# Optimization experiments

Hardware: AMD Instinct MI355X
Metric: run time of the kernel (lower is better)

The kernel has to match this reference:

```python
import jax, jax.numpy as jnp
import numpy as np
import math

B, NQ, NS, K = 4, 4096, 16384, 16
P, IN, D = 3, 128, 256
H = D // 16   # nhead = out_dim // 16 = 16
HD = D // H   # head_dim = 16
RADIUS = 4.0
EPS = 1e-5


def _ln(x, g, b):
    m = jnp.mean(x, -1, keepdims=True)
    v = jnp.mean((x - m) ** 2, -1, keepdims=True)
    return (x - m) / jnp.sqrt(v + EPS) * g + b


def _pos_enc(x, W_pos, b_pos):
    # LearnablePositionalEncoding: cat([x, cos(Linear(2*pi*x))], -1)
    return jnp.concatenate([x, jnp.cos((2.0 * math.pi * x) @ W_pos + b_pos)], axis=-1)


def setup_inputs() -> dict:
    key = jax.random.key(0)
    ks = jax.random.split(key, 24)
    f32 = jnp.float32

    def w(k, shape):
        return jax.random.uniform(k, shape, f32, -1.0, 1.0) / np.float32(np.sqrt(shape[0]))

    inp = {}
    inp['q_pts'] = jax.random.normal(ks[0], (B, NQ, P), f32)
    inp['s_pts'] = jax.random.normal(ks[1], (B, NS, P), f32)
    inp['src_feats'] = jax.random.normal(ks[2], (B, NS, IN), f32)
    inp['query_feats'] = jax.random.normal(ks[3], (B, NQ, IN), f32)
    # shared proj (in_dim != out_dim, skip_dim=None -> skip_proj is the same Linear)
    inp['W_proj'] = w(ks[4], (IN, D)); inp['b_proj'] = jnp.zeros((D,), f32)
    # positional encoding Linear(p_dim, out_dim - p_dim)
    inp['W_pos'] = w(ks[5], (P, D - P)); inp['b_pos'] = jnp.zeros((D - P,), f32)
    # TransformerDecoderLayer (norm_first) params
    inp['ln1_g'] = jnp.ones((D,), f32); inp['ln1_b'] = jnp.zeros((D,), f32)
    inp['sa_Wv'] = w(ks[6], (D, D)); inp['sa_bv'] = jnp.zeros((D,), f32)
    inp['sa_Wo'] = w(ks[7], (D, D)); inp['sa_bo'] = jnp.zeros((D,), f32)
    inp['ln2_g'] = jnp.ones((D,), f32); inp['ln2_b'] = jnp.zeros((D,), f32)
    inp['ca_Wq'] = w(ks[8], (D, D)); inp['ca_bq'] = jnp.zeros((D,), f32)
    inp['ca_Wk'] = w(ks[9], (D, D)); inp['ca_bk'] = jnp.zeros((D,), f32)
    inp['ca_Wv'] = w(ks[10], (D, D)); inp['ca_bv'] = jnp.zeros((D,), f32)
    inp['ca_Wo'] = w(ks[11], (D, D)); inp['ca_bo'] = jnp.zeros((D,), f32)
    inp['ln3_g'] = jnp.ones((D,), f32); inp['ln3_b'] = jnp.zeros((D,), f32)
    inp['W1'] = w(ks[12], (D, D)); inp['b1'] = jnp.zeros((D,), f32)
    inp['W2'] = w(ks[13], (D, D)); inp['b2'] = jnp.zeros((D,), f32)
    inp['neighb_inds'] = jax.random.randint(ks[14], (B, NQ, K), 0, NS)
    return inp


def reference(q_pts, s_pts, src_feats, query_feats, W_proj, b_proj, W_pos, b_pos,
              ln1_g, ln1_b, sa_Wv, sa_bv, sa_Wo, sa_bo, ln2_g, ln2_b,
              ca_Wq, ca_bq, ca_Wk, ca_bk, ca_Wv, ca_bv, ca_Wo, ca_bo,
              ln3_g, ln3_b, W1, b1, W2, b2, neighb_inds):
    # append shadow point at 1e6 with zero feature row
    s_pts_ = jnp.concatenate([s_pts, jnp.full_like(s_pts[:, :1, :], 1e6)], axis=1)   # [B,NS+1,P]
    src_ = jnp.concatenate([src_feats, jnp.zeros_like(src_feats[:, :1, :])], axis=1)  # [B,NS+1,IN]
    src_p = src_ @ W_proj + b_proj            # proj(src_feats)  [B,NS+1,D]
    qf = query_feats @ W_proj + b_proj        # skip_proj == proj (skip_dim=None)
    inds = neighb_inds % (NS + 1)
    flat = inds.reshape(B, -1, 1)             # [B, NQ*K, 1]
    neighbors = jnp.take_along_axis(s_pts_, jnp.broadcast_to(flat, (B, NQ * K, P)), axis=1).reshape(B, NQ, K, P)
    neighb_x = jnp.take_along_axis(src_p, jnp.broadcast_to(flat, (B, NQ * K, D)), axis=1).reshape(B, NQ, K, D)
    neighbors = neighbors - q_pts[:, :, None, :]
    neighb_x = neighb_x + _pos_enc(neighbors / RADIUS, W_pos, b_pos)
    query_x = qf + _pos_enc(jnp.zeros_like(q_pts), W_pos, b_pos)
    mask = jnp.linalg.norm(neighbors, axis=-1) > RADIUS   # [B,NQ,K], True = invalid key

    x = query_x   # [B,NQ,D]: a length-1 target sequence per query point
    # --- self-attention block (seq len 1 -> softmax == 1 -> only V/O projections matter) ---
    h = _ln(x, ln1_g, ln1_b)
    x = x + (h @ sa_Wv + sa_bv) @ sa_Wo + sa_bo
    # --- cross-attention to K gathered neighbors ---
    h = _ln(x, ln2_g, ln2_b)
    q = (h @ ca_Wq + ca_bq).reshape(B, NQ, H, HD)
    kk = (neighb_x @ ca_Wk + ca_bk).reshape(B, NQ, K, H, HD)
    vv = (neighb_x @ ca_Wv + ca_bv).reshape(B, NQ, K, H, HD)
    scores = jnp.einsum('bnhd,bnkhd->bnhk', q, kk) / np.float32(np.sqrt(HD))
    scores = jnp.where(mask[:, :, None, :], jnp.float32(-1e9), scores)
    att = jax.nn.softmax(scores, axis=-1)
    ctx = jnp.einsum('bnhk,bnkhd->bnhd', att, vv).reshape(B, NQ, D)
    x = x + ctx @ ca_Wo + ca_bo
    # --- feed-forward (dim_feedforward == d_model, relu) ---
    h = _ln(x, ln3_g, ln3_b)
    x = x + jax.nn.relu(h @ W1 + b1) @ W2 + b2
    # original zeroes any NaNs (fully-masked rows); shapes chosen so this is a no-op
    return jnp.nan_to_num(x)
```

## Files before the change

kernel.cpp:

```cpp
#include <hip/hip_runtime.h>
#include <hip/hip_bf16.h>
#include <math.h>
#include <stdint.h>

typedef __attribute__((ext_vector_type(8))) short short8;
typedef __attribute__((ext_vector_type(4))) float floatx4;

#define DEVI __device__ __forceinline__

DEVI float b2f(unsigned short u) {
    union { unsigned int i; float f; } v; v.i = ((unsigned int)u) << 16; return v.f;
}
DEVI unsigned short f2b(float f) {
    unsigned int x = __float_as_uint(f);
    unsigned int r = (x + 0x7fffu + ((x >> 16) & 1u)) >> 16;
    return (unsigned short)r;
}

#define GLD16(gp, lp)                                                            \
    __builtin_amdgcn_global_load_lds(                                            \
        (__attribute__((address_space(1))) unsigned int*)(gp),                   \
        (__attribute__((address_space(3))) unsigned int*)(lp), 16, 0, 0)

static constexpr int NQ = 4096, NS = 16384;
static constexpr int NROW_Q = 4 * NQ;
static constexpr int NROW_S = 4 * NS;
static constexpr float INV2PI = 0.15915494309189535f;

__global__ void k_prep(const float* Wproj, const float* saWv, const float* saWo,
                       const float* caWq, const float* caWk, const float* caWv,
                       const float* caWo, const float* W1, const float* W2,
                       const float* b_pos,
                       unsigned short* wTproj, unsigned short* wTsaWv, unsigned short* wTsaWo,
                       unsigned short* wTcaWq, unsigned short* wTkv, unsigned short* wTcaWo,
                       unsigned short* wTW1, unsigned short* wTW2, float* penc0)
{
    int z = blockIdx.z;
    if (z == 9) {
        if (blockIdx.x == 0 && blockIdx.y == 0) {
            int c = threadIdx.y * 16 + threadIdx.x;
            float v = 0.f;
            if (c >= 3) {
                float rev = b_pos[c - 3] * INV2PI;
                rev -= floorf(rev);
                v = __builtin_amdgcn_cosf(rev);
            }
            penc0[c] = v;
        }
        return;
    }
    int n = blockIdx.x * 16 + threadIdx.x;
    int k = blockIdx.y * 16 + threadIdx.y;
    const float* src; unsigned short* dst; int K = 256;
    switch (z) {
        case 0: src = Wproj; dst = wTproj; K = 128; break;
        case 1: src = saWv;  dst = wTsaWv; break;
        case 2: src = saWo;  dst = wTsaWo; break;
        case 3: src = caWq;  dst = wTcaWq; break;
        case 4: src = caWk;  dst = wTkv;   break;
        case 5: src = caWv;  dst = wTkv + 256 * 256; break;
        case 6: src = caWo;  dst = wTcaWo; break;
        case 7: src = W1;    dst = wTW1;   break;
        default: src = W2;   dst = wTW2;   break;
    }
    if (k < K) dst[(size_t)n * K + k] = f2b(src[(size_t)k * 256 + n]);
}

__global__ void k_cvt(const float* in, unsigned short* out, int n4)
{
    int i = blockIdx.x * blockDim.x + threadIdx.x;
    int stride = gridDim.x * blockDim.x;
    for (; i < n4; i += stride) {
        float4 v = ((const float4*)in)[i];
        unsigned long long p =
              (unsigned long long)f2b(v.x)
            | ((unsigned long long)f2b(v.y) << 16)
            | ((unsigned long long)f2b(v.z) << 32)
            | ((unsigned long long)f2b(v.w) << 48);
        ((unsigned long long*)out)[i] = p;
    }
}

template<int EPI>
__global__ __launch_bounds__(256, 2)
void k_gemm(const unsigned short* A, const unsigned short* BT, const float* bias,
            const float* extra, void* outp, int M, int N, int K)
{
    __shared__ alignas(16) unsigned short lA[128 * 64];
    __shared__ alignas(16) unsigned short lB[64 * 64];
    const int tid = threadIdx.x;
    const int wave = tid >> 6, lane = tid & 63;
    const int m0 = blockIdx.x * 128, n0 = blockIdx.y * 64;
    const int wm = (wave >> 1) * 64, wn = (wave & 1) * 32;
    floatx4 acc[4][2] = {};

    for (int kt = 0; kt < K; kt += 64) {
        __syncthreads();
        #pragma unroll
        for (int c = 0; c < 4; ++c) {
            int o = (tid + c * 256) * 16;
            int row = o >> 7, inner = o & 127;
            int srk = inner ^ ((row & 7) << 4);
            GLD16((const char*)A + ((size_t)(m0 + row) * K + kt) * 2 + srk, (char*)lA + o);
        }
        #pragma unroll
        for (int c = 0; c < 2; ++c) {
            int o = (tid + c * 256) * 16;
            int row = o >> 7, inner = o & 127;
            int srk = inner ^ ((row & 7) << 4);
            GLD16((const char*)BT + ((size_t)(n0 + row) * K + kt) * 2 + srk, (char*)lB + o);
        }
        __syncthreads();
        #pragma unroll
        for (int kc = 0; kc < 2; ++kc) {
            const int kb = kc * 64 + ((lane >> 4) << 4);
            short8 bf[2];
            #pragma unroll
            for (int nf = 0; nf < 2; ++nf) {
                int nn = wn + nf * 16 + (lane & 15);
                bf[nf] = *(const short8*)((const char*)lB + nn * 128 + (kb ^ ((nn & 7) << 4)));
            }
            #pragma unroll
            for (int mf = 0; mf < 4; ++mf) {
                int rr = wm + mf * 16 + (lane & 15);
                short8 af = *(const short8*)((const char*)lA + rr * 128 + (kb ^ ((rr & 7) << 4)));
                acc[mf][0] = __builtin_amdgcn_mfma_f32_16x16x32_bf16(af, bf[0], acc[mf][0], 0, 0, 0);
                acc[mf][1] = __builtin_amdgcn_mfma_f32_16x16x32_bf16(af, bf[1], acc[mf][1], 0, 0, 0);
            }
        }
    }
    #pragma unroll
    for (int mf = 0; mf < 4; ++mf)
        #pragma unroll
        for (int nf = 0; nf < 2; ++nf)
            #pragma unroll
            for (int r = 0; r < 4; ++r) {
                int row = m0 + wm + mf * 16 + ((lane >> 4) << 2) + r;
                int col = n0 + wn + nf * 16 + (lane & 15);
                float v = acc[mf][nf][r] + bias[col];
                if (EPI == 2) v += extra[col];
                if (EPI == 3 || EPI == 4) v += extra[(size_t)row * N + col];
                if (EPI == 1) v = fmaxf(v, 0.f);
                if (EPI == 4) {
                    if (isnan(v)) v = 0.f;
                    else if (isinf(v)) v = v > 0.f ? 3.402823466e38f : -3.402823466e38f;
                }
                if (EPI == 0 || EPI == 1)
                    ((unsigned short*)outp)[(size_t)row * N + col] = f2b(v);
                else
                    ((float*)outp)[(size_t)row * N + col] = v;
            }
}

__global__ __launch_bounds__(256, 2)
void k_ln(const float* x, const float* g, const float* b, unsigned short* out)
{
    int row = blockIdx.x * 4 + (threadIdx.x >> 6);
    int lane = threadIdx.x & 63;
    const float* xr = x + (size_t)row * 256;
    float4 v = ((const float4*)xr)[lane];
    float s = v.x + v.y + v.z + v.w;
    #pragma unroll
    for (int t = 32; t >= 1; t >>= 1) s += __shfl_xor(s, t, 64);
    float mean = s * (1.f / 256.f);
    float d0 = v.x - mean, d1 = v.y - mean, d2 = v.z - mean, d3 = v.w - mean;
    float q = d0 * d0 + d1 * d1 + d2 * d2 + d3 * d3;
    #pragma unroll
    for (int t = 32; t >= 1; t >>= 1) q += __shfl_xor(q, t, 64);
    float inv = 1.0f / sqrtf(q * (1.f / 256.f) + 1e-5f);
    int c = lane * 4;
    unsigned long long p =
          (unsigned long long)f2b(d0 * inv * g[c] + b[c])
        | ((unsigned long long)f2b(d1 * inv * g[c + 1] + b[c + 1]) << 16)
        | ((unsigned long long)f2b(d2 * inv * g[c + 2] + b[c + 2]) << 32)
        | ((unsigned long long)f2b(d3 * inv * g[c + 3] + b[c + 3]) << 48);
    ((unsigned long long*)(out + (size_t)row * 256))[lane] = p;
}

__global__ __launch_bounds__(256, 3)
void k_attn(const unsigned short* srcp, const unsigned short* qb, const int* inds,
            const float* s_pts, const float* q_pts, const float* W_pos, const float* b_pos,
            const unsigned short* wTkv, const float* bv, unsigned short* ctx)
{
    __shared__ alignas(16) unsigned short nx[64 * 256];
    __shared__ alignas(16) float att_lds[4 * 16 * 16];
    __shared__ alignas(16) float dist_lds[64];
    const int tid = threadIdx.x, wave = tid >> 6, lane = tid & 63;
    const int qbase = blockIdx.x * 4;
    const int l15 = lane & 15, lg = lane >> 4;

    {
        int r = tid >> 2, sub = tid & 3;
        int qi = qbase + (r >> 4);
        int bb = qi >> 12;
        int k = r & 15;
        int raw = inds[((size_t)qi << 4) + k];
        int idx = raw % (NS + 1); if (idx < 0) idx += NS + 1;
        bool shadow = (idx == NS);
        const int c0 = sub * 64;
        const unsigned short* srow = srcp + ((size_t)bb * NS + (shadow ? 0 : idx)) * 256 + c0;
        short8 sv[8];
        #pragma unroll
        for (int j = 0; j < 8; ++j) sv[j] = *(const short8*)(srow + j * 8);

        float px = q_pts[(size_t)qi * 3], py = q_pts[(size_t)qi * 3 + 1], pz = q_pts[(size_t)qi * 3 + 2];
        float sx, sy, sz;
        if (shadow) { sx = sy = sz = 1e6f; }
        else {
            const float* sp = s_pts + ((size_t)bb * NS + idx) * 3;
            sx = sp[0]; sy = sp[1]; sz = sp[2];
        }
        float tx = (sx - px) * 0.25f, ty = (sy - py) * 0.25f, tz = (sz - pz) * 0.25f;
        if (sub == 0) dist_lds[r] = tx * tx + ty * ty + tz * tz;

        #pragma unroll
        for (int cc = 0; cc < 64; cc += 8) {
            short8 vals;
            #pragma unroll
            for (int j = 0; j < 8; ++j) {
                int c = c0 + cc + j;
                float pe;
                if (c == 0) pe = tx;
                else if (c == 1) pe = ty;
                else if (c == 2) pe = tz;
                else {
                    int jj = c - 3;
                    float rev = fmaf(tx, W_pos[jj],
                                fmaf(ty, W_pos[253 + jj],
                                fmaf(tz, W_pos[506 + jj], b_pos[jj] * INV2PI)));
                    rev -= floorf(rev);
                    pe = __builtin_amdgcn_cosf(rev);
                }
                float sval = shadow ? 0.f : b2f((unsigned short)sv[cc / 8][j]);
                vals[j] = (short)f2b(sval + pe);
            }
            int byte = (c0 + cc) * 2;
            *(short8*)((char*)nx + r * 512 + (byte ^ ((r & 7) << 4))) = vals;
        }
    }
    __syncthreads();

    const int wn = wave * 64;
    floatx4 acc[4][4];

    #pragma unroll
    for (int mf = 0; mf < 4; ++mf)
        #pragma unroll
        for (int nf = 0; nf < 4; ++nf) acc[mf][nf] = floatx4{0.f, 0.f, 0.f, 0.f};

    #pragma unroll 2
    for (int kt = 0; kt < 8; ++kt) {
        const int kb = kt * 64 + (lg << 4);
        short8 bfr[4];
        #pragma unroll
        for (int nf = 0; nf < 4; ++nf) {
            int nn = wn + nf * 16 + l15;
            bfr[nf] = *(const short8*)((const char*)wTkv + (size_t)nn * 512 + kt * 64 + (lg << 4));
        }
        #pragma unroll
        for (int mf = 0; mf < 4; ++mf) {
            int rr = mf * 16 + l15;
            short8 af = *(const short8*)((const char*)nx + rr * 512 + (kb ^ ((rr & 7) << 4)));
            #pragma unroll
            for (int nf = 0; nf < 4; ++nf)
                acc[mf][nf] = __builtin_amdgcn_mfma_f32_16x16x32_bf16(af, bfr[nf], acc[mf][nf], 0, 0, 0);
        }
    }

    {
        #pragma unroll
        for (int mf = 0; mf < 4; ++mf) {
            float4 d4 = *(const float4*)&dist_lds[mf * 16 + lg * 4];
            float dd4[4] = {d4.x, d4.y, d4.z, d4.w};
            #pragma unroll
            for (int nf = 0; nf < 4; ++nf) {
                float qv = b2f(qb[(size_t)(qbase + mf) * 256 + (wave * 4 + nf) * 16 + l15]);
                float s[4];
                #pragma unroll
                for (int r = 0; r < 4; ++r) s[r] = acc[mf][nf][r] * qv;
                #pragma unroll
                for (int t = 1; t <= 8; t <<= 1)
                    #pragma unroll
                    for (int r = 0; r < 4; ++r) s[r] += __shfl_xor(s[r], t);
                #pragma unroll
                for (int r = 0; r < 4; ++r)
                    s[r] = (dd4[r] > 1.0f) ? -1e9f : s[r] * 0.25f;
                float m = fmaxf(fmaxf(s[0], s[1]), fmaxf(s[2], s[3]));
                m = fmaxf(m, __shfl_xor(m, 16));
                m = fmaxf(m, __shfl_xor(m, 32));
                float p[4], su = 0.f;
                #pragma unroll
                for (int r = 0; r < 4; ++r) { p[r] = __expf(s[r] - m); su += p[r]; }
                su += __shfl_xor(su, 16);
                su += __shfl_xor(su, 32);
                float inv = __builtin_amdgcn_rcpf(su);
                if (l15 == 0) {
                    float4 a4 = {p[0] * inv, p[1] * inv, p[2] * inv, p[3] * inv};
                    *(float4*)&att_lds[(mf * 16 + wave * 4 + nf) * 16 + lg * 4] = a4;
                }
            }
        }
    }

    #pragma unroll
    for (int mf = 0; mf < 4; ++mf)
        #pragma unroll
        for (int nf = 0; nf < 4; ++nf) acc[mf][nf] = floatx4{0.f, 0.f, 0.f, 0.f};

    #pragma unroll 2
    for (int kt = 0; kt < 8; ++kt) {
        const int kb = kt * 64 + (lg << 4);
        short8 bfr[4];
        #pragma unroll
        for (int nf = 0; nf < 4; ++nf) {
            int nn = 256 + wn + nf * 16 + l15;
            bfr[nf] = *(const short8*)((const char*)wTkv + (size_t)nn * 512 + kt * 64 + (lg << 4));
        }
        #pragma unroll
        for (int mf = 0; mf < 4; ++mf) {
            int rr = mf * 16 + l15;
            short8 af = *(const short8*)((const char*)nx + rr * 512 + (kb ^ ((rr & 7) << 4)));
            #pragma unroll
            for (int nf = 0; nf < 4; ++nf)
                acc[mf][nf] = __builtin_amdgcn_mfma_f32_16x16x32_bf16(af, bfr[nf], acc[mf][nf], 0, 0, 0);
        }
    }

    {
        #pragma unroll
        for (int mf = 0; mf < 4; ++mf)
            #pragma unroll
            for (int nf = 0; nf < 4; ++nf) {
                float4 a4 = *(const float4*)&att_lds[(mf * 16 + wave * 4 + nf) * 16 + lg * 4];
                float o = a4.x * acc[mf][nf][0];
                o = fmaf(a4.y, acc[mf][nf][1], o);
                o = fmaf(a4.z, acc[mf][nf][2], o);
                o = fmaf(a4.w, acc[mf][nf][3], o);
                o += __shfl_xor(o, 16);
                o += __shfl_xor(o, 32);
                o += bv[(wave * 4 + nf) * 16 + l15];
                if (lane < 16)
                    ctx[(size_t)(qbase + mf) * 256 + (wave * 4 + nf) * 16 + lane] = f2b(o);
            }
    }
}

extern "C" void kernel_launch(void* const* d_in, const int* in_sizes, int n_in,
                              void* d_out, int out_size, void* d_ws, size_t ws_size,
                              hipStream_t stream)
{
    const float* q_pts   = (const float*)d_in[0];
    const float* s_pts   = (const float*)d_in[1];
    const float* src_f   = (const float*)d_in[2];
    const float* query_f = (const float*)d_in[3];
    const float* W_proj  = (const float*)d_in[4];
    const float* b_proj  = (const float*)d_in[5];
    const float* W_pos   = (const float*)d_in[6];
    const float* b_pos   = (const float*)d_in[7];
    const float* ln1_g   = (const float*)d_in[8];
    const float* ln1_b   = (const float*)d_in[9];
    const float* sa_Wv   = (const float*)d_in[10];
    const float* sa_bv   = (const float*)d_in[11];
    const float* sa_Wo   = (const float*)d_in[12];
    const float* sa_bo   = (const float*)d_in[13];
    const float* ln2_g   = (const float*)d_in[14];
    const float* ln2_b   = (const float*)d_in[15];
    const float* ca_Wq   = (const float*)d_in[16];
    const float* ca_bq   = (const float*)d_in[17];
    const float* ca_Wk   = (const float*)d_in[18];
    const float* ca_Wv   = (const float*)d_in[20];
    const float* ca_bv   = (const float*)d_in[21];
    const float* ca_Wo   = (const float*)d_in[22];
    const float* ca_bo   = (const float*)d_in[23];
    const float* ln3_g   = (const float*)d_in[24];
    const float* ln3_b   = (const float*)d_in[25];
    const float* W1      = (const float*)d_in[26];
    const float* b1      = (const float*)d_in[27];
    const float* W2      = (const float*)d_in[28];
    const float* b2      = (const float*)d_in[29];
    const int*   inds    = (const int*)d_in[30];

    char* ws = (char*)d_ws;
    size_t off = 0;
    auto alloc = [&](size_t bytes) { char* p = ws + off; off += (bytes + 1023) & ~(size_t)1023; return p; };

    unsigned short* wTproj = (unsigned short*)alloc(256 * 128 * 2);
    unsigned short* wTsaWv = (unsigned short*)alloc(256 * 256 * 2);
    unsigned short* wTsaWo = (unsigned short*)alloc(256 * 256 * 2);
    unsigned short* wTcaWq = (unsigned short*)alloc(256 * 256 * 2);
    unsigned short* wTkv   = (unsigned short*)alloc(512 * 256 * 2);
    unsigned short* wTcaWo = (unsigned short*)alloc(256 * 256 * 2);
    unsigned short* wTW1   = (unsigned short*)alloc(256 * 256 * 2);
    unsigned short* wTW2   = (unsigned short*)alloc(256 * 256 * 2);
    float*          penc0  = (float*)alloc(256 * 4);
    unsigned short* srcb   = (unsigned short*)alloc((size_t)NROW_S * 128 * 2);
    unsigned short* qfb    = (unsigned short*)alloc((size_t)NROW_Q * 128 * 2);
    unsigned short* srcp   = (unsigned short*)alloc((size_t)NROW_S * 256 * 2);
    float*          qx     = (float*)alloc((size_t)NROW_Q * 256 * 4);
    unsigned short* hbuf   = (unsigned short*)alloc((size_t)NROW_Q * 256 * 2);
    unsigned short* tbuf   = (unsigned short*)alloc((size_t)NROW_Q * 256 * 2);
    float*          xbuf   = (float*)alloc((size_t)NROW_Q * 256 * 4);
    unsigned short* qbuf   = (unsigned short*)alloc((size_t)NROW_Q * 256 * 2);
    unsigned short* ctxbuf = (unsigned short*)alloc((size_t)NROW_Q * 256 * 2);
    float*          x2buf  = (float*)alloc((size_t)NROW_Q * 256 * 4);

    dim3 bl16(16, 16);
    k_prep<<<dim3(16, 16, 10), bl16, 0, stream>>>(
        W_proj, sa_Wv, sa_Wo, ca_Wq, ca_Wk, ca_Wv, ca_Wo, W1, W2, b_pos,
        wTproj, wTsaWv, wTsaWo, wTcaWq, wTkv, wTcaWo, wTW1, wTW2, penc0);

    k_cvt<<<1024, 256, 0, stream>>>(src_f, srcb, NROW_S * 128 / 4);
    k_cvt<<<1024, 256, 0, stream>>>(query_f, qfb, NROW_Q * 128 / 4);

    k_gemm<0><<<dim3(512, 4), 256, 0, stream>>>(srcb, wTproj, b_proj, nullptr, srcp, NROW_S, 256, 128);
    k_gemm<2><<<dim3(128, 4), 256, 0, stream>>>(qfb, wTproj, b_proj, penc0, qx, NROW_Q, 256, 128);

    k_ln<<<4096, 256, 0, stream>>>(qx, ln1_g, ln1_b, hbuf);
    k_gemm<0><<<dim3(128, 4), 256, 0, stream>>>(hbuf, wTsaWv, sa_bv, nullptr, tbuf, NROW_Q, 256, 256);
    k_gemm<3><<<dim3(128, 4), 256, 0, stream>>>(tbuf, wTsaWo, sa_bo, qx, xbuf, NROW_Q, 256, 256);

    k_ln<<<4096, 256, 0, stream>>>(xbuf, ln2_g, ln2_b, hbuf);
    k_gemm<0><<<dim3(128, 4), 256, 0, stream>>>(hbuf, wTcaWq, ca_bq, nullptr, qbuf, NROW_Q, 256, 256);
    k_attn<<<4096, 256, 0, stream>>>(srcp, qbuf, inds, s_pts, q_pts, W_pos, b_pos, wTkv, ca_bv, ctxbuf);
    k_gemm<3><<<dim3(128, 4), 256, 0, stream>>>(ctxbuf, wTcaWo, ca_bo, xbuf, x2buf, NROW_Q, 256, 256);

    k_ln<<<4096, 256, 0, stream>>>(x2buf, ln3_g, ln3_b, hbuf);
    k_gemm<1><<<dim3(128, 4), 256, 0, stream>>>(hbuf, wTW1, b1, nullptr, tbuf, NROW_Q, 256, 256);
    k_gemm<4><<<dim3(128, 4), 256, 0, stream>>>(tbuf, wTW2, b2, x2buf, d_out, NROW_Q, 256, 256);

    (void)in_sizes; (void)n_in; (void)out_size; (void)ws_size;
}
```

Baseline: 395.7 us.

## Make attention kernel persistent over four query groups with software-prefetched gathers

```diff
diff --git a/kernel.cpp b/kernel.cpp
--- a/kernel.cpp
+++ b/kernel.cpp
@@ -21,6 +21,10 @@
     __builtin_amdgcn_global_load_lds(                                            \
         (__attribute__((address_space(1))) unsigned int*)(gp),                   \
         (__attribute__((address_space(3))) unsigned int*)(lp), 16, 0, 0)
+
+#define BAR_LGKM()                                                               \
+    do { asm volatile("s_waitcnt lgkmcnt(0)" ::: "memory");                      \
+         __builtin_amdgcn_s_barrier(); } while (0)
 
 static constexpr int NQ = 4096, NS = 16384;
 static constexpr int NROW_Q = 4 * NQ;
@@ -64,6 +68,12 @@
         default: src = W2;   dst = wTW2;   break;
     }
     if (k < K) dst[(size_t)n * K + k] = f2b(src[(size_t)k * 256 + n]);
+}
+
+__global__ void k_scale(const float* b_pos, float* bp2)
+{
+    int i = blockIdx.x * blockDim.x + threadIdx.x;
+    if (i < 253) bp2[i] = b_pos[i] * INV2PI;
 }
 
 __global__ void k_cvt(const float* in, unsigned short* out, int n4)
@@ -179,30 +189,32 @@
 
 __global__ __launch_bounds__(256, 3)
 void k_attn(const unsigned short* srcp, const unsigned short* qb, const int* inds,
-            const float* s_pts, const float* q_pts, const float* W_pos, const float* b_pos,
+            const float* s_pts, const float* q_pts, const float* W_pos, const float* bp2,
             const unsigned short* wTkv, const float* bv, unsigned short* ctx)
 {
     __shared__ alignas(16) unsigned short nx[64 * 256];
     __shared__ alignas(16) float att_lds[4 * 16 * 16];
     __shared__ alignas(16) float dist_lds[64];
     const int tid = threadIdx.x, wave = tid >> 6, lane = tid & 63;
-    const int qbase = blockIdx.x * 4;
     const int l15 = lane & 15, lg = lane >> 4;
-
-    {
-        int r = tid >> 2, sub = tid & 3;
-        int qi = qbase + (r >> 4);
+    const int r = tid >> 2, sub = tid & 3;
+    const int c0 = sub * 64;
+    constexpr int NG = 4;
+
+    short8 sv[8];
+    float tx, ty, tz;
+    int shadow;
+
+    auto prefetch = [&](int g) {
+        int qi = (blockIdx.x * NG + g) * 4 + (r >> 4);
         int bb = qi >> 12;
         int k = r & 15;
         int raw = inds[((size_t)qi << 4) + k];
         int idx = raw % (NS + 1); if (idx < 0) idx += NS + 1;
-        bool shadow = (idx == NS);
-        const int c0 = sub * 64;
+        shadow = (idx == NS);
         const unsigned short* srow = srcp + ((size_t)bb * NS + (shadow ? 0 : idx)) * 256 + c0;
-        short8 sv[8];
         #pragma unroll
         for (int j = 0; j < 8; ++j) sv[j] = *(const short8*)(srow + j * 8);
-
         float px = q_pts[(size_t)qi * 3], py = q_pts[(size_t)qi * 3 + 1], pz = q_pts[(size_t)qi * 3 + 2];
         float sx, sy, sz;
         if (shadow) { sx = sy = sz = 1e6f; }
@@ -210,12 +222,14 @@
             const float* sp = s_pts + ((size_t)bb * NS + idx) * 3;
             sx = sp[0]; sy = sp[1]; sz = sp[2];
         }
-        float tx = (sx - px) * 0.25f, ty = (sy - py) * 0.25f, tz = (sz - pz) * 0.25f;
+        tx = (sx - px) * 0.25f; ty = (sy - py) * 0.25f; tz = (sz - pz) * 0.25f;
+    };
+
+    auto write_nx = [&]() {
         if (sub == 0) dist_lds[r] = tx * tx + ty * ty + tz * tz;
-
         #pragma unroll
         for (int cc = 0; cc < 64; cc += 8) {
-            short8 vals;
+            float f[8];
             #pragma unroll
             for (int j = 0; j < 8; ++j) {
                 int c = c0 + cc + j;
@@ -225,123 +239,136 @@
                 else if (c == 2) pe = tz;
                 else {
                     int jj = c - 3;
-                    float rev = fmaf(tx, W_pos[jj],
-                                fmaf(ty, W_pos[253 + jj],
-                                fmaf(tz, W_pos[506 + jj], b_pos[jj] * INV2PI)));
+                    float rev = fmaf(tx, W_pos[jj], fmaf(ty, W_pos[253 + jj], fmaf(tz, W_pos[506 + jj], bp2[jj])));
                     rev -= floorf(rev);
                     pe = __builtin_amdgcn_cosf(rev);
                 }
-                float sval = shadow ? 0.f : b2f((unsigned short)sv[cc / 8][j]);
-                vals[j] = (short)f2b(sval + pe);
-            }
+                f[j] = (shadow ? 0.f : b2f((unsigned short)sv[cc / 8][j])) + pe;
+            }
+            unsigned int w0, w1, w2, w3;
+            asm("v_cvt_pk_bf16_f32 %0, %1, %2" : "=v"(w0) : "v"(f[0]), "v"(f[1]));
+            asm("v_cvt_pk_bf16_f32 %0, %1, %2" : "=v"(w1) : "v"(f[2]), "v"(f[3]));
+            asm("v_cvt_pk_bf16_f32 %0, %1, %2" : "=v"(w2) : "v"(f[4]), "v"(f[5]));
+            asm("v_cvt_pk_bf16_f32 %0, %1, %2" : "=v"(w3) : "v"(f[6]), "v"(f[7]));
             int byte = (c0 + cc) * 2;
-            *(short8*)((char*)nx + r * 512 + (byte ^ ((r & 7) << 4))) = vals;
-        }
-    }
-    __syncthreads();
+            *(uint4*)((char*)nx + r * 512 + (byte ^ ((r & 7) << 4))) = make_uint4(w0, w1, w2, w3);
+        }
+    };
 
     const int wn = wave * 64;
-    floatx4 acc[4][4];
-
-    #pragma unroll
-    for (int mf = 0; mf < 4; ++mf)
-        #pragma unroll
-        for (int nf = 0; nf < 4; ++nf) acc[mf][nf] = floatx4{0.f, 0.f, 0.f, 0.f};
-
-    #pragma unroll 2
-    for (int kt = 0; kt < 8; ++kt) {
-        const int kb = kt * 64 + (lg << 4);
-        short8 bfr[4];
-        #pragma unroll
-        for (int nf = 0; nf < 4; ++nf) {
-            int nn = wn + nf * 16 + l15;
-            bfr[nf] = *(const short8*)((const char*)wTkv + (size_t)nn * 512 + kt * 64 + (lg << 4));
-        }
-        #pragma unroll
-        for (int mf = 0; mf < 4; ++mf) {
-            int rr = mf * 16 + l15;
-            short8 af = *(const short8*)((const char*)nx + rr * 512 + (kb ^ ((rr & 7) << 4)));
-            #pragma unroll
-            for (int nf = 0; nf < 4; ++nf)
-                acc[mf][nf] = __builtin_amdgcn_mfma_f32_16x16x32_bf16(af, bfr[nf], acc[mf][nf], 0, 0, 0);
-        }
-    }
-
-    {
-        #pragma unroll
-        for (int mf = 0; mf < 4; ++mf) {
-            float4 d4 = *(const float4*)&dist_lds[mf * 16 + lg * 4];
-            float dd4[4] = {d4.x, d4.y, d4.z, d4.w};
+
+    prefetch(0);
+    #pragma unroll 1
+    for (int g = 0; g < NG; ++g) {
+        const int qbase = (blockIdx.x * NG + g) * 4;
+
+        BAR_LGKM();
+        write_nx();
+        if (g + 1 < NG) prefetch(g + 1);
+        BAR_LGKM();
+
+        floatx4 acc[4][4];
+
+        #pragma unroll
+        for (int mf = 0; mf < 4; ++mf)
+            #pragma unroll
+            for (int nf = 0; nf < 4; ++nf) acc[mf][nf] = floatx4{0.f, 0.f, 0.f, 0.f};
+
+        #pragma unroll 2
+        for (int kt = 0; kt < 8; ++kt) {
+            const int kb = kt * 64 + (lg << 4);
+            short8 bfr[4];
             #pragma unroll
             for (int nf = 0; nf < 4; ++nf) {
-                float qv = b2f(qb[(size_t)(qbase + mf) * 256 + (wave * 4 + nf) * 16 + l15]);
-                float s[4];
+                int nn = wn + nf * 16 + l15;
+                bfr[nf] = *(const short8*)((const char*)wTkv + (size_t)nn * 512 + kt * 64 + (lg << 4));
+            }
+            #pragma unroll
+            for (int mf = 0; mf < 4; ++mf) {
+                int rr = mf * 16 + l15;
+                short8 af = *(const short8*)((const char*)nx + rr * 512 + (kb ^ ((rr & 7) << 4)));
                 #pragma unroll
-                for (int r = 0; r < 4; ++r) s[r] = acc[mf][nf][r] * qv;
+                for (int nf = 0; nf < 4; ++nf)
+                    acc[mf][nf] = __builtin_amdgcn_mfma_f32_16x16x32_bf16(af, bfr[nf], acc[mf][nf], 0, 0, 0);
+            }
+        }
+
+        {
+            #pragma unroll
+            for (int mf = 0; mf < 4; ++mf) {
+                float4 d4 = *(const float4*)&dist_lds[mf * 16 + lg * 4];
+                float dd4[4] = {d4.x, d4.y, d4.z, d4.w};
                 #pragma unroll
-                for (int t = 1; t <= 8; t <<= 1)
+                for (int nf = 0; nf < 4; ++nf) {
+                    float qv = b2f(qb[(size_t)(qbase + mf) * 256 + (wave * 4 + nf) * 16 + l15]);
+                    float s[4];
                     #pragma unroll
-                    for (int r = 0; r < 4; ++r) s[r] += __shfl_xor(s[r], t);
+                    for (int rr = 0; rr < 4; ++rr) s[rr] = acc[mf][nf][rr] * qv;
+                    #pragma unroll
+                    for (int t = 1; t <= 8; t <<= 1)
+                        #pragma unroll
+                        for (int rr = 0; rr < 4; ++rr) s[rr] += __shfl_xor(s[rr], t);
+                    #pragma unroll
+                    for (int rr = 0; rr < 4; ++rr)
+                        s[rr] = (dd4[rr] > 1.0f) ? -1e9f : s[rr] * 0.25f;
+                    float m = fmaxf(fmaxf(s[0], s[1]), fmaxf(s[2], s[3]));
+                    m = fmaxf(m, __shfl_xor(m, 16));
+                    m = fmaxf(m, __shfl_xor(m, 32));
+                    float p[4], su = 0.f;
+                    #pragma unroll
+                    for (int rr = 0; rr < 4; ++rr) { p[rr] = __expf(s[rr] - m); su += p[rr]; }
+                    su += __shfl_xor(su, 16);
+                    su += __shfl_xor(su, 32);
+                    float inv = __builtin_amdgcn_rcpf(su);
+                    if (l15 == 0) {
+                        float4 a4 = {p[0] * inv, p[1] * inv, p[2] * inv, p[3] * inv};
+                        *(float4*)&att_lds[(mf * 16 + wave * 4 + nf) * 16 + lg * 4] = a4;
+                    }
+                }
+            }
+        }
+
+        #pragma unroll
+        for (int mf = 0; mf < 4; ++mf)
+            #pragma unroll
+            for (int nf = 0; nf < 4; ++nf) acc[mf][nf] = floatx4{0.f, 0.f, 0.f, 0.f};
+
+        #pragma unroll 2
+        for (int kt = 0; kt < 8; ++kt) {
+            const int kb = kt * 64 + (lg << 4);
+            short8 bfr[4];
+            #pragma unroll
+            for (int nf = 0; nf < 4; ++nf) {
+                int nn = 256 + wn + nf * 16 + l15;
+                bfr[nf] = *(const short8*)((const char*)wTkv + (size_t)nn * 512 + kt * 64 + (lg << 4));
+            }
+            #pragma unroll
+            for (int mf = 0; mf < 4; ++mf) {
+                int rr = mf * 16 + l15;
+                short8 af = *(const short8*)((const char*)nx + rr * 512 + (kb ^ ((rr & 7) << 4)));
                 #pragma unroll
-                for (int r = 0; r < 4; ++r)
-                    s[r] = (dd4[r] > 1.0f) ? -1e9f : s[r] * 0.25f;
-                float m = fmaxf(fmaxf(s[0], s[1]), fmaxf(s[2], s[3]));
-                m = fmaxf(m, __shfl_xor(m, 16));
-                m = fmaxf(m, __shfl_xor(m, 32));
-                float p[4], su = 0.f;
+                for (int nf = 0; nf < 4; ++nf)
+                    acc[mf][nf] = __builtin_amdgcn_mfma_f32_16x16x32_bf16(af, bfr[nf], acc[mf][nf], 0, 0, 0);
+            }
+        }
+
+        {
+            #pragma unroll
+            for (int mf = 0; mf < 4; ++mf)
                 #pragma unroll
-                for (int r = 0; r < 4; ++r) { p[r] = __expf(s[r] - m); su += p[r]; }
-                su += __shfl_xor(su, 16);
-                su += __shfl_xor(su, 32);
-                float inv = __builtin_amdgcn_rcpf(su);
-                if (l15 == 0) {
-                    float4 a4 = {p[0] * inv, p[1] * inv, p[2] * inv, p[3] * inv};
-                    *(float4*)&att_lds[(mf * 16 + wave * 4 + nf) * 16 + lg * 4] = a4;
+                for (int nf = 0; nf < 4; ++nf) {
+                    float4 a4 = *(const float4*)&att_lds[(mf * 16 + wave * 4 + nf) * 16 + lg * 4];
+                    float o = a4.x * acc[mf][nf][0];
+                    o = fmaf(a4.y, acc[mf][nf][1], o);
+                    o = fmaf(a4.z, acc[mf][nf][2], o);
+                    o = fmaf(a4.w, acc[mf][nf][3], o);
+                    o += __shfl_xor(o, 16);
+                    o += __shfl_xor(o, 32);
+                    o += bv[(wave * 4 + nf) * 16 + l15];
+                    if (lane < 16)
+                        ctx[(size_t)(qbase + mf) * 256 + (wave * 4 + nf) * 16 + lane] = f2b(o);
                 }
-            }
-        }
-    }
-
-    #pragma unroll
-    for (int mf = 0; mf < 4; ++mf)
-        #pragma unroll
-        for (int nf = 0; nf < 4; ++nf) acc[mf][nf] = floatx4{0.f, 0.f, 0.f, 0.f};
-
-    #pragma unroll 2
-    for (int kt = 0; kt < 8; ++kt) {
-        const int kb = kt * 64 + (lg << 4);
-        short8 bfr[4];
-        #pragma unroll
-        for (int nf = 0; nf < 4; ++nf) {
-            int nn = 256 + wn + nf * 16 + l15;
-            bfr[nf] = *(const short8*)((const char*)wTkv + (size_t)nn * 512 + kt * 64 + (lg << 4));
-        }
-        #pragma unroll
-        for (int mf = 0; mf < 4; ++mf) {
-            int rr = mf * 16 + l15;
-            short8 af = *(const short8*)((const char*)nx + rr * 512 + (kb ^ ((rr & 7) << 4)));
-            #pragma unroll
-            for (int nf = 0; nf < 4; ++nf)
-                acc[mf][nf] = __builtin_amdgcn_mfma_f32_16x16x32_bf16(af, bfr[nf], acc[mf][nf], 0, 0, 0);
-        }
-    }
-
-    {
-        #pragma unroll
-        for (int mf = 0; mf < 4; ++mf)
-            #pragma unroll
-            for (int nf = 0; nf < 4; ++nf) {
-                float4 a4 = *(const float4*)&att_lds[(mf * 16 + wave * 4 + nf) * 16 + lg * 4];
-                float o = a4.x * acc[mf][nf][0];
-                o = fmaf(a4.y, acc[mf][nf][1], o);
-                o = fmaf(a4.z, acc[mf][nf][2], o);
-                o = fmaf(a4.w, acc[mf][nf][3], o);
-                o += __shfl_xor(o, 16);
-                o += __shfl_xor(o, 32);
-                o += bv[(wave * 4 + nf) * 16 + l15];
-                if (lane < 16)
-                    ctx[(size_t)(qbase + mf) * 256 + (wave * 4 + nf) * 16 + lane] = f2b(o);
-            }
+        }
     }
 }
 
@@ -393,6 +420,7 @@
     unsigned short* wTW1   = (unsigned short*)alloc(256 * 256 * 2);
     unsigned short* wTW2   = (unsigned short*)alloc(256 * 256 * 2);
     float*          penc0  = (float*)alloc(256 * 4);
+    float*          bp2    = (float*)alloc(256 * 4);
     unsigned short* srcb   = (unsigned short*)alloc((size_t)NROW_S * 128 * 2);
     unsigned short* qfb    = (unsigned short*)alloc((size_t)NROW_Q * 128 * 2);
     unsigned short* srcp   = (unsigned short*)alloc((size_t)NROW_S * 256 * 2);
@@ -408,6 +436,7 @@
     k_prep<<<dim3(16, 16, 10), bl16, 0, stream>>>(
         W_proj, sa_Wv, sa_Wo, ca_Wq, ca_Wk, ca_Wv, ca_Wo, W1, W2, b_pos,
         wTproj, wTsaWv, wTsaWo, wTcaWq, wTkv, wTcaWo, wTW1, wTW2, penc0);
+    k_scale<<<1, 256, 0, stream>>>(b_pos, bp2);
 
     k_cvt<<<1024, 256, 0, stream>>>(src_f, srcb, NROW_S * 128 / 4);
     k_cvt<<<1024, 256, 0, stream>>>(query_f, qfb, NROW_Q * 128 / 4);
@@ -421,7 +450,7 @@
 
     k_ln<<<4096, 256, 0, stream>>>(xbuf, ln2_g, ln2_b, hbuf);
     k_gemm<0><<<dim3(128, 4), 256, 0, stream>>>(hbuf, wTcaWq, ca_bq, nullptr, qbuf, NROW_Q, 256, 256);
-    k_attn<<<4096, 256, 0, stream>>>(srcp, qbuf, inds, s_pts, q_pts, W_pos, b_pos, wTkv, ca_bv, ctxbuf);
+    k_attn<<<1024, 256, 0, stream>>>(srcp, qbuf, inds, s_pts, q_pts, W_pos, bp2, wTkv, ca_bv, ctxbuf);
     k_gemm<3><<<dim3(128, 4), 256, 0, stream>>>(ctxbuf, wTcaWo, ca_bo, xbuf, x2buf, NROW_Q, 256, 256);
 
     k_ln<<<4096, 256, 0, stream>>>(x2buf, ln3_g, ln3_b, hbuf);
```

After: 457.5 us. 1.16x slower.

## Fuse LayerNorm into preceding GEMM epilogues with full-row tiles

Applied to the files above, without the earlier changes.

```diff
diff --git a/kernel.cpp b/kernel.cpp
--- a/kernel.cpp
+++ b/kernel.cpp
@@ -66,6 +66,12 @@
     if (k < K) dst[(size_t)n * K + k] = f2b(src[(size_t)k * 256 + n]);
 }
 
+__global__ void k_scale(const float* b_pos, float* bp2)
+{
+    int i = blockIdx.x * blockDim.x + threadIdx.x;
+    if (i < 253) bp2[i] = b_pos[i] * INV2PI;
+}
+
 __global__ void k_cvt(const float* in, unsigned short* out, int n4)
 {
     int i = blockIdx.x * blockDim.x + threadIdx.x;
@@ -138,8 +144,7 @@
                 int row = m0 + wm + mf * 16 + ((lane >> 4) << 2) + r;
                 int col = n0 + wn + nf * 16 + (lane & 15);
                 float v = acc[mf][nf][r] + bias[col];
-                if (EPI == 2) v += extra[col];
-                if (EPI == 3 || EPI == 4) v += extra[(size_t)row * N + col];
+                if (EPI == 4) v += extra[(size_t)row * N + col];
                 if (EPI == 1) v = fmaxf(v, 0.f);
                 if (EPI == 4) {
                     if (isnan(v)) v = 0.f;
@@ -152,34 +157,94 @@
             }
 }
 
+template<int EPI2>
 __global__ __launch_bounds__(256, 2)
-void k_ln(const float* x, const float* g, const float* b, unsigned short* out)
-{
-    int row = blockIdx.x * 4 + (threadIdx.x >> 6);
-    int lane = threadIdx.x & 63;
-    const float* xr = x + (size_t)row * 256;
-    float4 v = ((const float4*)xr)[lane];
-    float s = v.x + v.y + v.z + v.w;
-    #pragma unroll
-    for (int t = 32; t >= 1; t >>= 1) s += __shfl_xor(s, t, 64);
-    float mean = s * (1.f / 256.f);
-    float d0 = v.x - mean, d1 = v.y - mean, d2 = v.z - mean, d3 = v.w - mean;
-    float q = d0 * d0 + d1 * d1 + d2 * d2 + d3 * d3;
-    #pragma unroll
-    for (int t = 32; t >= 1; t >>= 1) q += __shfl_xor(q, t, 64);
-    float inv = 1.0f / sqrtf(q * (1.f / 256.f) + 1e-5f);
-    int c = lane * 4;
-    unsigned long long p =
-          (unsigned long long)f2b(d0 * inv * g[c] + b[c])
-        | ((unsigned long long)f2b(d1 * inv * g[c + 1] + b[c + 1]) << 16)
-        | ((unsigned long long)f2b(d2 * inv * g[c + 2] + b[c + 2]) << 32)
-        | ((unsigned long long)f2b(d3 * inv * g[c + 3] + b[c + 3]) << 48);
-    ((unsigned long long*)(out + (size_t)row * 256))[lane] = p;
+void k_gemm_ln(const unsigned short* A, const unsigned short* BT, const float* bias,
+               const float* extra, const float* lng, const float* lnb,
+               float* outf, unsigned short* outb, int M, int K)
+{
+    __shared__ alignas(16) unsigned short lA[64 * 64];
+    __shared__ alignas(16) unsigned short lB[256 * 64];
+    const int tid = threadIdx.x, wave = tid >> 6, lane = tid & 63;
+    const int l15 = lane & 15, lg = lane >> 4;
+    const int m0 = blockIdx.x * 64;
+    floatx4 acc[16] = {};
+
+    for (int kt = 0; kt < K; kt += 64) {
+        __syncthreads();
+        #pragma unroll
+        for (int c = 0; c < 2; ++c) {
+            int o = (tid + c * 256) * 16;
+            int row = o >> 7, inner = o & 127;
+            int srk = inner ^ ((row & 7) << 4);
+            GLD16((const char*)A + ((size_t)(m0 + row) * K + kt) * 2 + srk, (char*)lA + o);
+        }
+        #pragma unroll
+        for (int c = 0; c < 8; ++c) {
+            int o = (tid + c * 256) * 16;
+            int row = o >> 7, inner = o & 127;
+            int srk = inner ^ ((row & 7) << 4);
+            GLD16((const char*)BT + ((size_t)row * K + kt) * 2 + srk, (char*)lB + o);
+        }
+        __syncthreads();
+        #pragma unroll
+        for (int kc = 0; kc < 2; ++kc) {
+            const int kb = kc * 64 + (lg << 4);
+            int rr = wave * 16 + l15;
+            short8 af = *(const short8*)((const char*)lA + rr * 128 + (kb ^ ((rr & 7) << 4)));
+            #pragma unroll
+            for (int nf = 0; nf < 16; ++nf) {
+                int nn = nf * 16 + l15;
+                short8 bf = *(const short8*)((const char*)lB + nn * 128 + (kb ^ ((nn & 7) << 4)));
+                acc[nf] = __builtin_amdgcn_mfma_f32_16x16x32_bf16(af, bf, acc[nf], 0, 0, 0);
+            }
+        }
+    }
+
+    #pragma unroll
+    for (int nf = 0; nf < 16; ++nf) {
+        int col = nf * 16 + l15;
+        float bi = bias[col] + (EPI2 == 0 ? extra[col] : 0.f);
+        #pragma unroll
+        for (int r = 0; r < 4; ++r) {
+            int row = m0 + wave * 16 + lg * 4 + r;
+            float v = acc[nf][r] + bi;
+            if (EPI2 == 1) v += extra[(size_t)row * 256 + col];
+            acc[nf][r] = v;
+            outf[(size_t)row * 256 + col] = v;
+        }
+    }
+    float mean[4], inv[4];
+    #pragma unroll
+    for (int r = 0; r < 4; ++r) {
+        float s = 0.f;
+        #pragma unroll
+        for (int nf = 0; nf < 16; ++nf) s += acc[nf][r];
+        #pragma unroll
+        for (int t = 1; t <= 8; t <<= 1) s += __shfl_xor(s, t);
+        mean[r] = s * (1.f / 256.f);
+        float q = 0.f;
+        #pragma unroll
+        for (int nf = 0; nf < 16; ++nf) { float d = acc[nf][r] - mean[r]; q += d * d; }
+        #pragma unroll
+        for (int t = 1; t <= 8; t <<= 1) q += __shfl_xor(q, t);
+        inv[r] = 1.0f / sqrtf(q * (1.f / 256.f) + 1e-5f);
+    }
+    #pragma unroll
+    for (int nf = 0; nf < 16; ++nf) {
+        int col = nf * 16 + l15;
+        float g = lng[col], b = lnb[col];
+        #pragma unroll
+        for (int r = 0; r < 4; ++r) {
+            int row = m0 + wave * 16 + lg * 4 + r;
+            outb[(size_t)row * 256 + col] = f2b((acc[nf][r] - mean[r]) * inv[r] * g + b);
+        }
+    }
 }
 
 __global__ __launch_bounds__(256, 3)
 void k_attn(const unsigned short* srcp, const unsigned short* qb, const int* inds,
-            const float* s_pts, const float* q_pts, const float* W_pos, const float* b_pos,
+            const float* s_pts, const float* q_pts, const float* W_pos, const float* bp2,
             const unsigned short* wTkv, const float* bv, unsigned short* ctx)
 {
     __shared__ alignas(16) unsigned short nx[64 * 256];
@@ -188,6 +253,15 @@
     const int tid = threadIdx.x, wave = tid >> 6, lane = tid & 63;
     const int qbase = blockIdx.x * 4;
     const int l15 = lane & 15, lg = lane >> 4;
+
+    float qv[4][4], bvv[4];
+    #pragma unroll
+    for (int mf = 0; mf < 4; ++mf)
+        #pragma unroll
+        for (int nf = 0; nf < 4; ++nf)
+            qv[mf][nf] = b2f(qb[(size_t)(qbase + mf) * 256 + (wave * 4 + nf) * 16 + l15]) * 0.25f;
+    #pragma unroll
+    for (int nf = 0; nf < 4; ++nf) bvv[nf] = bv[(wave * 4 + nf) * 16 + l15];
 
     {
         int r = tid >> 2, sub = tid & 3;
@@ -227,7 +301,7 @@
                     int jj = c - 3;
                     float rev = fmaf(tx, W_pos[jj],
                                 fmaf(ty, W_pos[253 + jj],
-                                fmaf(tz, W_pos[506 + jj], b_pos[jj] * INV2PI)));
+                                fmaf(tz, W_pos[506 + jj], bp2[jj])));
                     rev -= floorf(rev);
                     pe = __builtin_amdgcn_cosf(rev);
                 }
@@ -274,23 +348,22 @@
             float dd4[4] = {d4.x, d4.y, d4.z, d4.w};
             #pragma unroll
             for (int nf = 0; nf < 4; ++nf) {
-                float qv = b2f(qb[(size_t)(qbase + mf) * 256 + (wave * 4 + nf) * 16 + l15]);
                 float s[4];
                 #pragma unroll
-                for (int r = 0; r < 4; ++r) s[r] = acc[mf][nf][r] * qv;
+                for (int rr = 0; rr < 4; ++rr) s[rr] = acc[mf][nf][rr] * qv[mf][nf];
                 #pragma unroll
                 for (int t = 1; t <= 8; t <<= 1)
                     #pragma unroll
-                    for (int r = 0; r < 4; ++r) s[r] += __shfl_xor(s[r], t);
+                    for (int rr = 0; rr < 4; ++rr) s[rr] += __shfl_xor(s[rr], t);
                 #pragma unroll
-                for (int r = 0; r < 4; ++r)
-                    s[r] = (dd4[r] > 1.0f) ? -1e9f : s[r] * 0.25f;
+                for (int rr = 0; rr < 4; ++rr)
+                    s[rr] = (dd4[rr] > 1.0f) ? -1e9f : s[rr];
                 float m = fmaxf(fmaxf(s[0], s[1]), fmaxf(s[2], s[3]));
                 m = fmaxf(m, __shfl_xor(m, 16));
                 m = fmaxf(m, __shfl_xor(m, 32));
                 float p[4], su = 0.f;
                 #pragma unroll
-                for (int r = 0; r < 4; ++r) { p[r] = __expf(s[r] - m); su += p[r]; }
+                for (int rr = 0; rr < 4; ++rr) { p[rr] = __expf(s[rr] - m); su += p[rr]; }
                 su += __shfl_xor(su, 16);
                 su += __shfl_xor(su, 32);
                 float inv = __builtin_amdgcn_rcpf(su);
@@ -338,7 +411,7 @@
                 o = fmaf(a4.w, acc[mf][nf][3], o);
                 o += __shfl_xor(o, 16);
                 o += __shfl_xor(o, 32);
-                o += bv[(wave * 4 + nf) * 16 + l15];
+                o += bvv[nf];
                 if (lane < 16)
                     ctx[(size_t)(qbase + mf) * 256 + (wave * 4 + nf) * 16 + lane] = f2b(o);
             }
@@ -393,6 +466,7 @@
     unsigned short* wTW1   = (unsigned short*)alloc(256 * 256 * 2);
     unsigned short* wTW2   = (unsigned short*)alloc(256 * 256 * 2);
     float*          penc0  = (float*)alloc(256 * 4);
+    float*          bp2    = (float*)alloc(256 * 4);
     unsigned short* srcb   = (unsigned short*)alloc((size_t)NROW_S * 128 * 2);
     unsigned short* qfb    = (unsigned short*)alloc((size_t)NROW_Q * 128 * 2);
     unsigned short* srcp   = (unsigned short*)alloc((size_t)NROW_S * 256 * 2);
@@ -408,23 +482,24 @@
     k_prep<<<dim3(16, 16, 10), bl16, 0, stream>>>(
         W_proj, sa_Wv, sa_Wo, ca_Wq, ca_Wk, ca_Wv, ca_Wo, W1, W2, b_pos,
         wTproj, wTsaWv, wTsaWo, wTcaWq, wTkv, wTcaWo, wTW1, wTW2, penc0);
+    k_scale<<<1, 256, 0, stream>>>(b_pos, bp2);
 
     k_cvt<<<1024, 256, 0, stream>>>(src_f, srcb, NROW_S * 128 / 4);
     k_cvt<<<1024, 256, 0, stream>>>(query_f, qfb, NROW_Q * 128 / 4);
 
     k_gemm<0><<<dim3(512, 4), 256, 0, stream>>>(srcb, wTproj, b_proj, nullptr, srcp, NROW_S, 256, 128);
-    k_gemm<2><<<dim3(128, 4), 256, 0, stream>>>(qfb, wTproj, b_proj, penc0, qx, NROW_Q, 256, 128);
-
-    k_ln<<<4096, 256, 0, stream>>>(qx, ln1_g, ln1_b, hbuf);
+    k_gemm_ln<0><<<256, 256, 0, stream>>>(qfb, wTproj, b_proj, penc0, ln1_g, ln1_b,
+                                          qx, hbuf, NROW_Q, 128);
+
     k_gemm<0><<<dim3(128, 4), 256, 0, stream>>>(hbuf, wTsaWv, sa_bv, nullptr, tbuf, NROW_Q, 256, 256);
-    k_gemm<3><<<dim3(128, 4), 256, 0, stream>>>(tbuf, wTsaWo, sa_bo, qx, xbuf, NROW_Q, 256, 256);
-
-    k_ln<<<4096, 256, 0, stream>>>(xbuf, ln2_g, ln2_b, hbuf);
+    k_gemm_ln<1><<<256, 256, 0, stream>>>(tbuf, wTsaWo, sa_bo, qx, ln2_g, ln2_b,
+                                          xbuf, hbuf, NROW_Q, 256);
+
     k_gemm<0><<<dim3(128, 4), 256, 0, stream>>>(hbuf, wTcaWq, ca_bq, nullptr, qbuf, NROW_Q, 256, 256);
-    k_attn<<<4096, 256, 0, stream>>>(srcp, qbuf, inds, s_pts, q_pts, W_pos, b_pos, wTkv, ca_bv, ctxbuf);
-    k_gemm<3><<<dim3(128, 4), 256, 0, stream>>>(ctxbuf, wTcaWo, ca_bo, xbuf, x2buf, NROW_Q, 256, 256);
-
-    k_ln<<<4096, 256, 0, stream>>>(x2buf, ln3_g, ln3_b, hbuf);
+    k_attn<<<4096, 256, 0, stream>>>(srcp, qbuf, inds, s_pts, q_pts, W_pos, bp2, wTkv, ca_bv, ctxbuf);
+    k_gemm_ln<1><<<256, 256, 0, stream>>>(ctxbuf, wTcaWo, ca_bo, xbuf, ln3_g, ln3_b,
+                                          x2buf, hbuf, NROW_Q, 256);
+
     k_gemm<1><<<dim3(128, 4), 256, 0, stream>>>(hbuf, wTW1, b1, nullptr, tbuf, NROW_Q, 256, 256);
     k_gemm<4><<<dim3(128, 4), 256, 0, stream>>>(tbuf, wTW2, b2, x2buf, d_out, NROW_Q, 256, 256);
 
```

Measured after the change: 394.2 us. About the same (-0.4%).
